# Kernel optimization log

Hardware: AMD Instinct MI355X
Metric: run time of the kernel (lower is better)

The kernel has to match this reference:

```python
import jax, jax.numpy as jnp
import numpy as np

# ---- static physical configuration (matches init_kwargs param dict) ----
NX = NY = 513
NL = 3
N_ENS = 4
LX = LY = 5120.0e3
DX = LX / (NX - 1)
DY = LY / (NY - 1)
F0 = 9.375e-5
BETA = 1.754e-11
A2 = 0.0
A4 = 2.0e9
DELTA_EK = 2.0
TAU0 = 2.0e-5
BCCO = 0.2
ZFBC = BCCO / (1.0 + 0.5 * BCCO)
DT = 600.0
NUM_STEPS = 4
HEIGHTS = np.array([350.0, 750.0, 2900.0])
RED_G = np.array([0.025, 0.0125])

JAC_COEF = 1.0 / (F0 * DX * DY)
HYPERDIFF_COEF = A4 / F0**2 / DX**6
BOTTOM_FRICTION_COEF = DELTA_EK / (2.0 * abs(F0) * DX**2 * (-HEIGHTS[-1]))


def _build_constants():
    """Precompute stratification / mode / Helmholtz matrices (float64 numpy, cast to f32)."""
    A = np.zeros((NL, NL))
    A[0, 0] = 1.0 / (HEIGHTS[0] * RED_G[0])
    A[0, 1] = -1.0 / (HEIGHTS[0] * RED_G[0])
    for i in range(1, NL - 1):
        A[i, i - 1] = -1.0 / (HEIGHTS[i] * RED_G[i - 1])
        A[i, i] = 1.0 / HEIGHTS[i] * (1.0 / RED_G[i] + 1.0 / RED_G[i - 1])
        A[i, i + 1] = -1.0 / (HEIGHTS[i] * RED_G[i])
    A[-1, -1] = 1.0 / (HEIGHTS[NL - 1] * RED_G[NL - 2])
    A[-1, -2] = -1.0 / (HEIGHTS[NL - 1] * RED_G[NL - 2])
    lam_r, R = np.linalg.eig(A)
    lam_l, L = np.linalg.eig(A.T)
    lam_r, R, lam_l, L = lam_r.real, R.real, lam_l.real, L.real
    # align left eigenvectors with right eigenvalue ordering (biorthogonality)
    order = np.array([int(np.argmin(np.abs(lam_l - lr))) for lr in lam_r])
    L = L[:, order]
    Cl2m = np.diag(1.0 / np.diag(L.T @ R)) @ L.T
    Cm2l = R
    lambd = lam_r
    # DST-I eigenvalues of the 5-point Laplacian on the interior grid
    xg, yg = np.meshgrid(np.arange(1, NX - 1), np.arange(1, NY - 1), indexing='ij')
    lap_dst = (2 * (np.cos(np.pi / (NX - 1) * xg) - 1) / DX**2
               + 2 * (np.cos(np.pi / (NY - 1) * yg) - 1) / DY**2)
    helm_dst = lap_dst[None] / F0**2 - lambd[:, None, None]  # (nl, nx-2, ny-2)

    def np_dstI1D(x):
        N = x.shape[-1]
        xp = np.zeros(x.shape[:-1] + (N + 2,))
        xp[..., 1:-1] = x
        return np.fft.irfft(-1j * xp, n=2 * (N + 1), axis=-1, norm='ortho')[..., 1:N + 1]

    def np_dstI2D(x):
        return np.swapaxes(np_dstI1D(np.swapaxes(np_dstI1D(x), -1, -2)), -1, -2)

    const = np.ones((NL, NX, NY)) / (NX * NY)
    s = np.zeros_like(const)
    s[:, 1:-1, 1:-1] = np_dstI2D(np_dstI2D(const[:, 1:-1, 1:-1]) / helm_dst)
    hom_sol = (const + s * lambd[:, None, None])[:-1]  # (nl-1, nx, ny)
    M = (Cm2l[1:] - Cm2l[:-1])[:NL - 1, :NL - 1] * hom_sol.mean((1, 2))[None, :]
    alpha = -np.linalg.inv(M) @ (Cm2l[1:, :-1] - Cm2l[:-1, :-1])
    # wind forcing: curl(tau)/(f0*H1) on interior points; tau_y = 0, tau_x(y) only
    tau_x = -TAU0 * np.cos(2 * np.pi * (np.arange(NY) + 0.5) / NY)[None, :] * np.ones((NX, NY))
    dtaux_dy = (tau_x[1:-1, 2:] - tau_x[1:-1, :-2]) / (2 * DY)
    wind = (-dtaux_dy / (F0 * HEIGHTS[0]))[None]  # (1, nx-2, ny-2)
    f32 = lambda a: jnp.asarray(a, jnp.float32)
    return dict(A=f32(A), Cl2m=f32(Cl2m), Cm2l=f32(Cm2l), helmoltz_dst=f32(helm_dst),
                alpha_matrix=f32(alpha), homogeneous_sol=f32(hom_sol), wind_forcing=f32(wind))


# ---------------- stencil ops ----------------

def _pad11(x):
    return jnp.pad(x, [(0, 0)] * (x.ndim - 2) + [(1, 1), (1, 1)])


def laplacian_h_nobc(f):
    # unscaled 5-point Laplacian, interior values only: (..., nx-2, ny-2)
    return (f[..., 2:, 1:-1] + f[..., :-2, 1:-1] + f[..., 1:-1, 2:] + f[..., 1:-1, :-2]
            - 4.0 * f[..., 1:-1, 1:-1])


def laplacian_h(f, fc):
    # full-grid Laplacian with partial-slip boundary treatment (coefficient fc = zfbc)
    lap = _pad11(laplacian_h_nobc(f))
    lap = lap.at[..., 0, :].set(fc * (f[..., 1, :] - f[..., 0, :]))
    lap = lap.at[..., -1, :].set(fc * (f[..., -2, :] - f[..., -1, :]))
    lap = lap.at[..., :, 0].set(fc * (f[..., :, 1] - f[..., :, 0]))
    lap = lap.at[..., :, -1].set(fc * (f[..., :, -2] - f[..., :, -1]))
    return lap


def laplacian_h_boundaries(f, fc):
    # boundary Laplacian values, concat order: x=0 (y interior), x=-1, y=0 (full x), y=-1
    return jnp.concatenate([
        fc * (f[..., 1, 1:-1] - f[..., 0, 1:-1]),
        fc * (f[..., -2, 1:-1] - f[..., -1, 1:-1]),
        fc * (f[..., :, 1] - f[..., :, 0]),
        fc * (f[..., :, -2] - f[..., :, -1])], axis=-1)


def jacobi_h(f, g):
    # Arakawa 9-point Jacobian J(f, g), interior values (..., nx-2, ny-2)
    dx_f = f[..., 2:, :] - f[..., :-2, :]
    dx_g = g[..., 2:, :] - g[..., :-2, :]
    dy_f = f[..., 2:] - f[..., :-2]
    dy_g = g[..., 2:] - g[..., :-2]
    return ((dx_f[..., 1:-1] * dy_g[..., 1:-1, :] - dx_g[..., 1:-1] * dy_f[..., 1:-1, :])
            + (f[..., 2:, 1:-1] * dy_g[..., 2:, :] - f[..., :-2, 1:-1] * dy_g[..., :-2, :])
            - (f[..., 1:-1, 2:] * dx_g[..., 2:] - f[..., 1:-1, :-2] * dx_g[..., :-2])
            + (g[..., 1:-1, 2:] * dx_f[..., 2:] - g[..., 1:-1, :-2] * dx_f[..., :-2])
            - (g[..., 2:, 1:-1] * dy_f[..., 2:, :] - g[..., :-2, 1:-1] * dy_f[..., :-2, :])) / 12.0


# ---------------- DST-I elliptic solve ----------------

def dstI1D(x):
    N = x.shape[-1]
    z = jnp.zeros(x.shape[:-1] + (1,), x.dtype)
    xp = jnp.concatenate([z, x, z], axis=-1)
    return jnp.fft.irfft(-1j * xp.astype(jnp.complex64), n=2 * (N + 1), axis=-1,
                         norm='ortho')[..., 1:N + 1]


def dstI2D(x):
    return jnp.swapaxes(dstI1D(jnp.swapaxes(dstI1D(x), -1, -2)), -1, -2)


def inverse_elliptic_dst(f, op_dst):
    return dstI2D(dstI2D(f) / op_dst)


# ---------------- QG time derivative ----------------

def _time_derivatives(y, A, Cl2m, Cm2l, helm_dst, alpha, hom_sol, wind):
    q, p = y[0], y[1]  # (..., nl, nx, ny)
    # advection + hyperdiffusion RHS on interior (a_2 == 0 branch skipped as in source)
    rhs = JAC_COEF * jacobi_h(q, p)
    delta2_p = laplacian_h(p, ZFBC)
    rhs = rhs - HYPERDIFF_COEF * laplacian_h_nobc(laplacian_h(delta2_p, ZFBC))
    rhs = rhs.at[..., 0:1, :, :].add(wind)
    rhs = rhs.at[..., -1:, :, :].add(BOTTOM_FRICTION_COEF * laplacian_h_nobc(p[..., -1:, :, :]))
    dq = _pad11(rhs)
    # layers -> modes, DST Helmholtz inversion, homogeneous-solution correction
    rhs_h = jnp.einsum('ij,...jxy->...ixy', Cl2m, dq)
    dp_modes = _pad11(inverse_elliptic_dst(rhs_h[..., 1:-1, 1:-1], helm_dst))
    mean_m = dp_modes[..., :-1, :, :].mean((-2, -1))  # (..., nl-1)
    dalpha = jnp.einsum('ij,...j->...i', alpha, mean_m)[..., None, None]
    dp_modes = dp_modes.at[..., :-1, :, :].add(dalpha * hom_sol)
    dp = jnp.einsum('ij,...jxy->...ixy', Cm2l, dp_modes)
    # boundary vorticity update
    dp_bound = jnp.concatenate([dp[..., 0, 1:-1], dp[..., -1, 1:-1],
                                dp[..., :, 0], dp[..., :, -1]], axis=-1)
    delta_p_bound = laplacian_h_boundaries(dp / (F0 * DX)**2, ZFBC)
    dq_bound = delta_p_bound - jnp.einsum('ij,...jl->...il', A, dp_bound)
    ny2 = NY - 2
    dq = dq.at[..., 0, 1:-1].set(dq_bound[..., :ny2])
    dq = dq.at[..., -1, 1:-1].set(dq_bound[..., ny2:2 * ny2])
    dq = dq.at[..., :, 0].set(dq_bound[..., 2 * ny2:2 * ny2 + NX])
    dq = dq.at[..., :, -1].set(dq_bound[..., 2 * ny2 + NX:2 * ny2 + 2 * NX])
    return jnp.stack((dq, dp), 0)


def _forecast(y0, t, A, Cl2m, Cm2l, helm_dst, alpha, hom_sol, wind):
    deriv = lambda y: _time_derivatives(y, A, Cl2m, Cm2l, helm_dst, alpha, hom_sol, wind)

    def step(y, dt_):
        k1 = deriv(y)
        k2 = deriv(y + 0.5 * dt_ * k1)
        k3 = deriv(y + 0.5 * dt_ * k2)
        k4 = deriv(y + dt_ * k3)
        y_next = y + (dt_ / 6.0) * (k1 + 2.0 * k2 + 2.0 * k3 + k4)
        return y_next, y_next

    _, traj = jax.lax.scan(step, y0, t[1:] - t[:-1])
    return jnp.concatenate([y0[None], traj], axis=0)  # (T, 2, n_ens, nl, nx, ny)


def setup_inputs() -> dict:
    key = jax.random.key(0)
    y0 = 0.1 * jax.random.normal(key, (2, N_ENS, NL, NX, NY), dtype=jnp.float32)
    t = jnp.arange(NUM_STEPS + 1, dtype=jnp.float32) * DT
    consts = _build_constants()
    return dict(y0=y0, t=t, **consts)


def reference(y0, t, A, Cl2m, Cm2l, helmoltz_dst, alpha_matrix, homogeneous_sol, wind_forcing):
    return _forecast(y0, t, A, Cl2m, Cm2l, helmoltz_dst, alpha_matrix,
                     homogeneous_sol, wind_forcing)
```

## Files before the change

### kernel.cpp

```cpp
#include <hip/hip_runtime.h>
#include <math.h>

#define NXY 513
#define NIN 511
#define NL3 3
#define NE4 4
#define NB 12
#define GLD 512

static constexpr long FS  = (long)NE4 * NL3 * NXY * NXY;
static constexpr long GSZ = (long)NB * GLD * GLD;
static constexpr int  NSTEPS = 4;

static constexpr double dF0 = 9.375e-05;
static constexpr double dDX = 10000.0;
static constexpr float ZFBCf     = (float)(0.2 / (1.0 + 0.5 * 0.2));
static constexpr float JACCf     = (float)(1.0 / (dF0 * dDX * dDX));
static constexpr float HYPCf     = (float)(2.0e9 / (dF0 * dF0) / (dDX*dDX*dDX*dDX*dDX*dDX));
static constexpr float BFCf      = (float)(2.0 / (2.0 * dF0 * dDX * dDX * (-2900.0)));
static constexpr float INVF0DX2f = (float)(1.0 / ((dF0 * dDX) * (dF0 * dDX)));

typedef short  bf16x8 __attribute__((ext_vector_type(8)));
typedef float  f32x4  __attribute__((ext_vector_type(4)));
typedef unsigned int u32;
typedef __attribute__((address_space(1))) const u32 GAS;
typedef __attribute__((address_space(3))) u32 LAS;
#define GLDS(gp, lp) __builtin_amdgcn_global_load_lds((GAS*)(gp), (LAS*)(lp), 16, 0, 0)

__device__ __forceinline__ unsigned short f2bf(float x) {
    unsigned int u = __float_as_uint(x);
    return (unsigned short)((u + 0x7FFFu + ((u >> 16) & 1u)) >> 16);
}
__device__ __forceinline__ float bf2f(unsigned short h) {
    return __uint_as_float(((unsigned int)h) << 16);
}

__global__ void initS_kernel(unsigned short* __restrict__ Sh, unsigned short* __restrict__ Sl) {
    int k = blockIdx.x * 256 + threadIdx.x;
    int n = blockIdx.y;
    if (k >= GLD || n >= GLD) return;
    float v = 0.f;
    if (n < NIN && k < NIN) {
        int m = ((n + 1) * (k + 1)) & 1023;
        v = (float)(0.0625 * sin(M_PI * (double)m / 512.0));
    }
    unsigned short hs = f2bf(v);
    Sh[n * GLD + k] = hs;
    Sl[n * GLD + k] = f2bf(v - bf2f(hs));
}

__global__ __launch_bounds__(256) void fused_rhs(
    float* __restrict__ kq, const float* __restrict__ q, const float* __restrict__ p,
    const float* __restrict__ wind)
{
    __shared__ float ps[22][72];
    __shared__ float qs[22][72];
    __shared__ float l1[22][72];
    __shared__ float l2[22][72];
    const int c  = blockIdx.z;
    const int x0 = 1 + blockIdx.y * 16;
    const int y0 = 1 + blockIdx.x * 64;
    const int t  = threadIdx.x;
    const size_t off = (size_t)c * NXY * NXY;
    const float* pp = p + off;
    const float* qp = q + off;

    for (int idx = t; idx < 22 * 70; idx += 256) {
        int i = idx / 70, j = idx % 70;
        int gx = x0 - 3 + i, gy = y0 - 3 + j;
        bool in = (gx >= 0 && gx < NXY && gy >= 0 && gy < NXY);
        size_t go = (size_t)gx * NXY + gy;
        ps[i][j] = in ? pp[go] : 0.f;
        qs[i][j] = in ? qp[go] : 0.f;
    }
    __syncthreads();

#define LAPBC(a, i, j, gx, gy) \
    ((gy) == 0       ? ZFBCf * (a[i][(j)+1] - a[i][j]) : \
     (gy) == NXY-1   ? ZFBCf * (a[i][(j)-1] - a[i][j]) : \
     (gx) == 0       ? ZFBCf * (a[(i)+1][j] - a[i][j]) : \
     (gx) == NXY-1   ? ZFBCf * (a[(i)-1][j] - a[i][j]) : \
     a[(i)+1][j] + a[(i)-1][j] + a[i][(j)+1] + a[i][(j)-1] - 4.f * a[i][j])

    for (int idx = t; idx < 20 * 68; idx += 256) {
        int i = 1 + idx / 68, j = 1 + idx % 68;
        int gx = x0 - 3 + i, gy = y0 - 3 + j;
        float v = 0.f;
        if (gx >= 0 && gx < NXY && gy >= 0 && gy < NXY) v = LAPBC(ps, i, j, gx, gy);
        l1[i][j] = v;
    }
    __syncthreads();

    for (int idx = t; idx < 18 * 66; idx += 256) {
        int i = 2 + idx / 66, j = 2 + idx % 66;
        int gx = x0 - 3 + i, gy = y0 - 3 + j;
        float v = 0.f;
        if (gx >= 0 && gx < NXY && gy >= 0 && gy < NXY) v = LAPBC(l1, i, j, gx, gy);
        l2[i][j] = v;
    }
    __syncthreads();
#undef LAPBC

    const int l = c % NL3;
    for (int idx = t; idx < 16 * 64; idx += 256) {
        int i = 3 + idx / 64, j = 3 + idx % 64;
        int gx = x0 - 3 + i, gy = y0 - 3 + j;
        if (gx > NIN || gy > NIN) continue;
        float fmm=qs[i-1][j-1], fm0=qs[i-1][j], fmp=qs[i-1][j+1];
        float f0m=qs[i][j-1],                    f0p=qs[i][j+1];
        float fpm=qs[i+1][j-1], fp0=qs[i+1][j], fpp=qs[i+1][j+1];
        float gmm=ps[i-1][j-1], gm0=ps[i-1][j], gmp=ps[i-1][j+1];
        float g0m=ps[i][j-1],   g00=ps[i][j],   g0p=ps[i][j+1];
        float gpm=ps[i+1][j-1], gp0=ps[i+1][j], gpp=ps[i+1][j+1];
        float J1 = (fp0 - fm0) * (g0p - g0m) - (gp0 - gm0) * (f0p - f0m);
        float J2 = fp0 * (gpp - gpm) - fm0 * (gmp - gmm);
        float J3 = f0p * (gpp - gmp) - f0m * (gpm - gmm);
        float J4 = g0p * (fpp - fmp) - g0m * (fpm - fmm);
        float J5 = gp0 * (fpp - fpm) - gm0 * (fmp - fmm);
        float jac = (J1 + J2 - J3 + J4 - J5) * (1.0f / 12.0f);
        float lap3 = l2[i+1][j] + l2[i-1][j] + l2[i][j+1] + l2[i][j-1] - 4.f * l2[i][j];
        float v = JACCf * jac - HYPCf * lap3;
        if (l == 0)       v += wind[(size_t)(gx-1) * NIN + (gy-1)];
        if (l == NL3-1)   v += BFCf * (gp0 + gm0 + g0p + g0m - 4.f * g00);
        kq[off + (size_t)gx * NXY + gy] = v;
    }
}

__global__ void l2m_kernel(unsigned short* __restrict__ Gh, unsigned short* __restrict__ Gl,
                           const float* __restrict__ kq, const float* __restrict__ Cl2m) {
    int ry = blockIdx.x * blockDim.x + threadIdx.x;
    int rx = blockIdx.y * blockDim.y + threadIdx.y;
    int e = blockIdx.z;
    size_t go = (size_t)(e * NL3) * GLD * GLD + (size_t)rx * GLD + ry;
    if (rx >= NIN || ry >= NIN) {
        for (int i = 0; i < 3; ++i) { Gh[go + (size_t)i*GLD*GLD] = 0; Gl[go + (size_t)i*GLD*GLD] = 0; }
        return;
    }
    size_t base = ((size_t)(e * NL3) * NXY + (rx + 1)) * NXY + (ry + 1);
    float f0 = kq[base];
    float f1 = kq[base + (size_t)NXY*NXY];
    float f2 = kq[base + 2*(size_t)NXY*NXY];
    float v[3];
    v[0] = Cl2m[0]*f0 + Cl2m[1]*f1 + Cl2m[2]*f2;
    v[1] = Cl2m[3]*f0 + Cl2m[4]*f1 + Cl2m[5]*f2;
    v[2] = Cl2m[6]*f0 + Cl2m[7]*f1 + Cl2m[8]*f2;
#pragma unroll
    for (int i = 0; i < 3; ++i) {
        unsigned short hs = f2bf(v[i]);
        Gh[go + (size_t)i*GLD*GLD] = hs;
        Gl[go + (size_t)i*GLD*GLD] = f2bf(v[i] - bf2f(hs));
    }
}

#define EPLD 133
__global__ __launch_bounds__(256, 2) void gemm_dst(
    const unsigned short* __restrict__ Ah, const unsigned short* __restrict__ Al,
    const unsigned short* __restrict__ Sh, const unsigned short* __restrict__ Sl,
    unsigned short* __restrict__ Ch, unsigned short* __restrict__ Cl,
    float* __restrict__ Cf, const float* __restrict__ helm)
{
    __shared__ __attribute__((aligned(16))) char ldsraw[49152];
    float* ep = (float*)ldsraw;
    const int id = blockIdx.x;
    const int nblk = id / 48, rr = id - nblk * 48;
    const int b = rr >> 2, mblk = rr & 3;
    const int m0 = mblk << 7, n0 = nblk << 6;
    const int t = threadIdx.x;
    const int wave = t >> 6, lane = t & 63;
    const int wr = wave >> 1, wc = wave & 1;
    const int lr = lane & 15, g = lane >> 4;
    const unsigned short* Abh = Ah + (size_t)b * 262144;
    const unsigned short* Abl = Al + (size_t)b * 262144;

    size_t gA[2]; int ldA[2];
#pragma unroll
    for (int u = 0; u < 2; ++u) {
        int o = wave*1024 + u*4096 + lane*16;
        gA[u] = (size_t)(m0 + (o >> 6)) * 512 + ((o & 63) >> 1);
        ldA[u] = wave*1024 + u*4096;
    }
    int oB = wave*1024 + lane*16;
    size_t gB = (size_t)(n0 + (oB >> 6)) * 512 + ((oB & 63) >> 1);
    int ldB = wave*1024;

    auto STAGE = [&](int buf, int kt) {
        char* bb = ldsraw + buf*24576;
        int ke = kt * 32;
#pragma unroll
        for (int u = 0; u < 2; ++u) {
            GLDS(Abh + gA[u] + ke, bb + ldA[u]);
            GLDS(Abl + gA[u] + ke, bb + 8192 + ldA[u]);
        }
        GLDS(Sh + gB + ke, bb + 16384 + ldB);
        GLDS(Sl + gB + ke, bb + 20480 + ldB);
    };

    f32x4 acc[4][2] = {};
    int abyte[4], bbyte[2];
#pragma unroll
    for (int i = 0; i < 4; ++i) abyte[i] = (wr*64 + i*16 + lr)*64 + g*16;
#pragma unroll
    for (int j = 0; j < 2; ++j) bbyte[j] = 16384 + (wc*32 + j*16 + lr)*64 + g*16;

    STAGE(0, 0);
    __syncthreads();
    for (int it = 0; it < 16; ++it) {
        const int buf = it & 1;
        if (it < 15) STAGE(buf ^ 1, it + 1);
        const char* bb = ldsraw + buf*24576;
        bf16x8 fbh[2], fbl[2];
#pragma unroll
        for (int j = 0; j < 2; ++j) {
            fbh[j] = *(const bf16x8*)(bb + bbyte[j]);
            fbl[j] = *(const bf16x8*)(bb + 4096 + bbyte[j]);
        }
#pragma unroll
        for (int i = 0; i < 4; ++i) {
            bf16x8 fah = *(const bf16x8*)(bb + abyte[i]);
            bf16x8 fal = *(const bf16x8*)(bb + 8192 + abyte[i]);
#pragma unroll
            for (int j = 0; j < 2; ++j) {
                acc[i][j] = __builtin_amdgcn_mfma_f32_16x16x32_bf16(fah, fbh[j], acc[i][j], 0, 0, 0);
                acc[i][j] = __builtin_amdgcn_mfma_f32_16x16x32_bf16(fah, fbl[j], acc[i][j], 0, 0, 0);
                acc[i][j] = __builtin_amdgcn_mfma_f32_16x16x32_bf16(fal, fbh[j], acc[i][j], 0, 0, 0);
            }
        }
        __syncthreads();
    }

    const int mode = b % NL3;
    const float* hp = helm ? (helm + (size_t)mode * NIN * NIN) : nullptr;
#pragma unroll
    for (int i = 0; i < 4; ++i) {
        int mml = wr*64 + i*16 + 4*g;
#pragma unroll
        for (int j = 0; j < 2; ++j) {
            int nnl = wc*32 + j*16 + lr;
            int nn = n0 + nnl;
            float v[4];
#pragma unroll
            for (int r = 0; r < 4; ++r) v[r] = acc[i][j][r];
            if (hp && nn < NIN) {
                int mmb = m0 + mml;
#pragma unroll
                for (int r = 0; r < 4; ++r)
                    if (mmb + r < NIN) v[r] /= hp[(size_t)nn*NIN + mmb + r];
            }
#pragma unroll
            for (int r = 0; r < 4; ++r) ep[nnl*EPLD + mml + r] = v[r];
        }
    }
    __syncthreads();

#pragma unroll
    for (int c = 0; c < 4; ++c) {
        int chunk = t + 256*c;
        int row = chunk >> 4;
        int cb  = (chunk & 15) * 8;
        float v[8];
#pragma unroll
        for (int k = 0; k < 8; ++k) v[k] = ep[row*EPLD + cb + k];
        size_t co = (size_t)b*262144 + (size_t)(n0 + row)*512 + m0 + cb;
        if (Cf) {
            f32x4 v0 = {v[0], v[1], v[2], v[3]};
            f32x4 v1 = {v[4], v[5], v[6], v[7]};
            *(f32x4*)(Cf + co)     = v0;
            *(f32x4*)(Cf + co + 4) = v1;
        } else {
            unsigned int h[4], lo[4];
#pragma unroll
            for (int k = 0; k < 4; ++k) {
                unsigned short h0 = f2bf(v[2*k]), h1 = f2bf(v[2*k+1]);
                unsigned short l0 = f2bf(v[2*k]-bf2f(h0)), l1 = f2bf(v[2*k+1]-bf2f(h1));
                h[k]  = (unsigned int)h0 | ((unsigned int)h1 << 16);
                lo[k] = (unsigned int)l0 | ((unsigned int)l1 << 16);
            }
            *(uint4*)(Ch + co) = make_uint4(h[0], h[1], h[2], h[3]);
            *(uint4*)(Cl + co) = make_uint4(lo[0], lo[1], lo[2], lo[3]);
        }
    }
}

__global__ void mean_kernel(float* __restrict__ partial, const float* __restrict__ G) {
    int gy = blockIdx.y;
    int e = gy >> 1, m = gy & 1;
    const float* g = G + (size_t)(e * NL3 + m) * GLD * GLD;
    float s = 0.f;
    for (int idx = blockIdx.x * 256 + threadIdx.x; idx < GLD*GLD; idx += 64 * 256)
        s += g[idx];
    __shared__ float red[256];
    red[threadIdx.x] = s; __syncthreads();
    for (int w = 128; w >= 1; w >>= 1) {
        if (threadIdx.x < w) red[threadIdx.x] += red[threadIdx.x + w];
        __syncthreads();
    }
    if (threadIdx.x == 0) partial[gy * 64 + blockIdx.x] = red[0];
}

__global__ void dalpha_kernel(float* __restrict__ dal, const float* __restrict__ partial,
                              const float* __restrict__ alpha) {
    int t = threadIdx.x;
    if (t >= 8) return;
    int e = t >> 1, i = t & 1;
    float s0 = 0.f, s1 = 0.f;
    for (int bk = 0; bk < 64; ++bk) { s0 += partial[(e*2+0)*64 + bk]; s1 += partial[(e*2+1)*64 + bk]; }
    const float inv = 1.0f / ((float)NXY * (float)NXY);
    dal[t] = alpha[i*2+0] * (s0 * inv) + alpha[i*2+1] * (s1 * inv);
}

__global__ void m2l_kernel(float* __restrict__ kp, const float* __restrict__ G,
                           const float* __restrict__ dal, const float* __restrict__ hom,
                           const float* __restrict__ Cm2l) {
    int y = blockIdx.x * blockDim.x + threadIdx.x;
    int x = blockIdx.y * blockDim.y + threadIdx.y;
    int e = blockIdx.z;
    if (x >= NXY || y >= NXY) return;
    float mv[3];
    bool interior = (x >= 1 && x <= NIN && y >= 1 && y <= NIN);
#pragma unroll
    for (int i = 0; i < 3; ++i)
        mv[i] = interior ? G[(size_t)(e*NL3 + i) * GLD * GLD + (size_t)(x-1) * GLD + (y-1)] : 0.f;
    float h0 = hom[(size_t)x * NXY + y];
    float h1 = hom[(size_t)NXY*NXY + (size_t)x * NXY + y];
    mv[0] += dal[e*2 + 0] * h0;
    mv[1] += dal[e*2 + 1] * h1;
#pragma unroll
    for (int l = 0; l < 3; ++l)
        kp[((size_t)(e*NL3 + l) * NXY + x) * NXY + y] =
            Cm2l[l*3+0]*mv[0] + Cm2l[l*3+1]*mv[1] + Cm2l[l*3+2]*mv[2];
}

__global__ void bound_kernel(float* __restrict__ kq, const float* __restrict__ kp,
                             const float* __restrict__ Amat) {
    int pos = blockIdx.x * 256 + threadIdx.x;
    int e = blockIdx.y;
    if (pos >= 2048) return;
    int x, y, xn, yn;
    if (pos < NIN)            { x = 0;      y = pos + 1;        xn = 1;      yn = y; }
    else if (pos < 2*NIN)     { x = NXY-1;  y = pos - NIN + 1;  xn = NXY-2;  yn = y; }
    else if (pos < 2*NIN+NXY) { x = pos - 2*NIN;       y = 0;      xn = x; yn = 1; }
    else                      { x = pos - (2*NIN+NXY); y = NXY-1;  xn = x; yn = NXY-2; }
    float dpb[3], lpb[3];
#pragma unroll
    for (int j = 0; j < 3; ++j) {
        const float* f = kp + (size_t)(e*NL3 + j) * NXY * NXY;
        float c = f[(size_t)x * NXY + y];
        float nb = f[(size_t)xn * NXY + yn];
        dpb[j] = c;
        lpb[j] = ZFBCf * INVF0DX2f * (nb - c);
    }
#pragma unroll
    for (int l = 0; l < 3; ++l) {
        float v = lpb[l] - (Amat[l*3+0]*dpb[0] + Amat[l*3+1]*dpb[1] + Amat[l*3+2]*dpb[2]);
        kq[((size_t)(e*NL3 + l) * NXY + x) * NXY + y] = v;
    }
}

__global__ void rk_fused(float4* __restrict__ o1, float4* __restrict__ o2,
                         const float4* __restrict__ x, const float4* __restrict__ k,
                         float c1, float c2, int accumulate,
                         const float* __restrict__ t, int s, long n4) {
    float dt = t[s+1] - t[s];
    float a1 = c1 * dt, a2 = c2 * dt;
    for (long i = (long)blockIdx.x * blockDim.x + threadIdx.x; i < n4;
         i += (long)gridDim.x * blockDim.x) {
        float4 kk = k[i], xx = x[i];
        float4 b0 = accumulate ? o1[i] : xx;
        o1[i] = make_float4(b0.x + a1*kk.x, b0.y + a1*kk.y, b0.z + a1*kk.z, b0.w + a1*kk.w);
        if (o2) o2[i] = make_float4(xx.x + a2*kk.x, xx.y + a2*kk.y, xx.z + a2*kk.z, xx.w + a2*kk.w);
    }
}

__global__ void copy_kernel(float4* __restrict__ out, const float4* __restrict__ in, long n4) {
    for (long i = (long)blockIdx.x * blockDim.x + threadIdx.x; i < n4;
         i += (long)gridDim.x * blockDim.x)
        out[i] = in[i];
}

extern "C" void kernel_launch(void* const* d_in, const int* in_sizes, int n_in,
                              void* d_out, int out_size, void* d_ws, size_t ws_size,
                              hipStream_t stream) {
    const float* y0    = (const float*)d_in[0];
    const float* tarr  = (const float*)d_in[1];
    const float* Amat  = (const float*)d_in[2];
    const float* Cl2m  = (const float*)d_in[3];
    const float* Cm2l  = (const float*)d_in[4];
    const float* helm  = (const float*)d_in[5];
    const float* alpha = (const float*)d_in[6];
    const float* hom   = (const float*)d_in[7];
    const float* wind  = (const float*)d_in[8];
    float* out = (float*)d_out;
    char* base = (char*)d_ws;

    unsigned short* Sh = (unsigned short*)base;
    unsigned short* Sl = (unsigned short*)(base + 512*1024);
    float* ytmp = (float*)(base + 1024*1024);
    float* kbuf = ytmp + 2*FS;
    char*  REGb = (char*)(kbuf + 2*FS);
    unsigned short* P0h = (unsigned short*)REGb;
    unsigned short* P0l = P0h + GSZ;
    unsigned short* P1h = P0l + GSZ;
    unsigned short* P1l = P1h + GSZ;
    float* R4 = (float*)REGb;
    float* partial = (float*)(REGb + (size_t)2*FS*sizeof(float));
    float* dal = partial + 512;

    const dim3 bSt(64, 4, 1);
    const dim3 gSt4((NXY + 63)/64, (NXY + 3)/4, NE4);
    const dim3 gL2M(8, 128, NE4);
    const dim3 gF(8, 32, NB);
    const dim3 gG(384, 1, 1);
    const long n4 = 2*FS/4;

    initS_kernel<<<dim3(2, GLD), 256, 0, stream>>>(Sh, Sl);
    copy_kernel<<<1024, 256, 0, stream>>>((float4*)out, (const float4*)y0, n4);

    auto deriv = [&](const float* y, float* k) {
        const float* q = y;  const float* p = y + FS;
        float* kq = k;       float* kp = k + FS;
        fused_rhs<<<gF, 256, 0, stream>>>(kq, q, p, wind);
        l2m_kernel<<<gL2M, bSt, 0, stream>>>(P0h, P0l, kq, Cl2m);
        gemm_dst<<<gG, 256, 0, stream>>>(P0h, P0l, Sh, Sl, P1h, P1l, nullptr, nullptr);
        gemm_dst<<<gG, 256, 0, stream>>>(P1h, P1l, Sh, Sl, P0h, P0l, nullptr, helm);
        gemm_dst<<<gG, 256, 0, stream>>>(P0h, P0l, Sh, Sl, P1h, P1l, nullptr, nullptr);
        gemm_dst<<<gG, 256, 0, stream>>>(P1h, P1l, Sh, Sl, nullptr, nullptr, R4, nullptr);
        mean_kernel<<<dim3(64, 8), 256, 0, stream>>>(partial, R4);
        dalpha_kernel<<<1, 64, 0, stream>>>(dal, partial, alpha);
        m2l_kernel<<<gSt4, bSt, 0, stream>>>(kp, R4, dal, hom, Cm2l);
        bound_kernel<<<dim3(8, NE4), 256, 0, stream>>>(kq, kp, Amat);
    };

    for (int s = 0; s < NSTEPS; ++s) {
        float* ycur  = out + (size_t)s * 2 * FS;
        float* ynext = out + (size_t)(s + 1) * 2 * FS;
        deriv(ycur, kbuf);
        rk_fused<<<1024, 256, 0, stream>>>((float4*)ynext, (float4*)ytmp, (const float4*)ycur,
                                           (const float4*)kbuf, 1.f/6.f, 0.5f, 0, tarr, s, n4);
        deriv(ytmp, kbuf);
        rk_fused<<<1024, 256, 0, stream>>>((float4*)ynext, (float4*)ytmp, (const float4*)ycur,
                                           (const float4*)kbuf, 2.f/6.f, 0.5f, 1, tarr, s, n4);
        deriv(ytmp, kbuf);
        rk_fused<<<1024, 256, 0, stream>>>((float4*)ynext, (float4*)ytmp, (const float4*)ycur,
                                           (const float4*)kbuf, 2.f/6.f, 1.0f, 1, tarr, s, n4);
        deriv(ytmp, kbuf);
        rk_fused<<<1024, 256, 0, stream>>>((float4*)ynext, nullptr, (const float4*)ycur,
                                           (const float4*)kbuf, 1.f/6.f, 0.f, 1, tarr, s, n4);
    }
}
```

Before: 2.283 ms.

## Shrink DST GEMM tile to 64x64 with XOR-swizzled LDS layout

The split-bf16 DST GEMM tile is halved from 128x64 to 64x64, doubling the grid to 768 blocks and cutting LDS per block to 32KB so launch bounds can request 3 blocks per SIMD. The LDS staging layout now uses an XOR swizzle on the 16-byte column chunk to reduce bank conflicts on fragment reads. This aims at better CU occupancy and fill across the 256 CUs, at the cost of less A/B reuse per block and more global traffic for the shared DST matrix.

```diff
diff --git a/kernel.cpp b/kernel.cpp
--- a/kernel.cpp
+++ b/kernel.cpp
@@ -152,19 +152,19 @@
     }
 }
 
-#define EPLD 133
-__global__ __launch_bounds__(256, 2) void gemm_dst(
+#define EPLD 68
+__global__ __launch_bounds__(256, 3) void gemm_dst(
     const unsigned short* __restrict__ Ah, const unsigned short* __restrict__ Al,
     const unsigned short* __restrict__ Sh, const unsigned short* __restrict__ Sl,
     unsigned short* __restrict__ Ch, unsigned short* __restrict__ Cl,
     float* __restrict__ Cf, const float* __restrict__ helm)
 {
-    __shared__ __attribute__((aligned(16))) char ldsraw[49152];
+    __shared__ __attribute__((aligned(16))) char ldsraw[32768];
     float* ep = (float*)ldsraw;
     const int id = blockIdx.x;
-    const int nblk = id / 48, rr = id - nblk * 48;
-    const int b = rr >> 2, mblk = rr & 3;
-    const int m0 = mblk << 7, n0 = nblk << 6;
+    const int nblk = id / 96, rr = id - nblk * 96;
+    const int b = rr >> 3, mblk = rr & 7;
+    const int m0 = mblk << 6, n0 = nblk << 6;
     const int t = threadIdx.x;
     const int wave = t >> 6, lane = t & 63;
     const int wr = wave >> 1, wc = wave & 1;
@@ -172,42 +172,40 @@
     const unsigned short* Abh = Ah + (size_t)b * 262144;
     const unsigned short* Abl = Al + (size_t)b * 262144;
 
-    size_t gA[2]; int ldA[2];
-#pragma unroll
-    for (int u = 0; u < 2; ++u) {
-        int o = wave*1024 + u*4096 + lane*16;
-        gA[u] = (size_t)(m0 + (o >> 6)) * 512 + ((o & 63) >> 1);
-        ldA[u] = wave*1024 + u*4096;
-    }
-    int oB = wave*1024 + lane*16;
-    size_t gB = (size_t)(n0 + (oB >> 6)) * 512 + ((oB & 63) >> 1);
-    int ldB = wave*1024;
+    const int srow = t >> 2;
+    const int scol = ((t & 3) ^ ((srow >> 1) & 3)) * 8;
+    const size_t gAe = (size_t)(m0 + srow) * 512 + scol;
+    const size_t gBe = (size_t)(n0 + srow) * 512 + scol;
+    const int ldbase = wave * 1024;
 
     auto STAGE = [&](int buf, int kt) {
-        char* bb = ldsraw + buf*24576;
+        char* bb = ldsraw + buf * 16384;
         int ke = kt * 32;
-#pragma unroll
-        for (int u = 0; u < 2; ++u) {
-            GLDS(Abh + gA[u] + ke, bb + ldA[u]);
-            GLDS(Abl + gA[u] + ke, bb + 8192 + ldA[u]);
-        }
-        GLDS(Sh + gB + ke, bb + 16384 + ldB);
-        GLDS(Sl + gB + ke, bb + 20480 + ldB);
+        GLDS(Abh + gAe + ke, bb + ldbase);
+        GLDS(Abl + gAe + ke, bb + 4096 + ldbase);
+        GLDS(Sh  + gBe + ke, bb + 8192 + ldbase);
+        GLDS(Sl  + gBe + ke, bb + 12288 + ldbase);
     };
 
-    f32x4 acc[4][2] = {};
-    int abyte[4], bbyte[2];
-#pragma unroll
-    for (int i = 0; i < 4; ++i) abyte[i] = (wr*64 + i*16 + lr)*64 + g*16;
-#pragma unroll
-    for (int j = 0; j < 2; ++j) bbyte[j] = 16384 + (wc*32 + j*16 + lr)*64 + g*16;
+    f32x4 acc[2][2] = {};
+    int abyte[2], bbyte[2];
+#pragma unroll
+    for (int i = 0; i < 2; ++i) {
+        int ar = wr*32 + i*16 + lr;
+        abyte[i] = ar*64 + ((g ^ ((ar >> 1) & 3)) * 16);
+    }
+#pragma unroll
+    for (int j = 0; j < 2; ++j) {
+        int br = wc*32 + j*16 + lr;
+        bbyte[j] = 8192 + br*64 + ((g ^ ((br >> 1) & 3)) * 16);
+    }
 
     STAGE(0, 0);
     __syncthreads();
     for (int it = 0; it < 16; ++it) {
         const int buf = it & 1;
         if (it < 15) STAGE(buf ^ 1, it + 1);
-        const char* bb = ldsraw + buf*24576;
+        const char* bb = ldsraw + buf * 16384;
         bf16x8 fbh[2], fbl[2];
 #pragma unroll
         for (int j = 0; j < 2; ++j) {
@@ -215,9 +213,9 @@
             fbl[j] = *(const bf16x8*)(bb + 4096 + bbyte[j]);
         }
 #pragma unroll
-        for (int i = 0; i < 4; ++i) {
+        for (int i = 0; i < 2; ++i) {
             bf16x8 fah = *(const bf16x8*)(bb + abyte[i]);
-            bf16x8 fal = *(const bf16x8*)(bb + 8192 + abyte[i]);
+            bf16x8 fal = *(const bf16x8*)(bb + 4096 + abyte[i]);
 #pragma unroll
             for (int j = 0; j < 2; ++j) {
                 acc[i][j] = __builtin_amdgcn_mfma_f32_16x16x32_bf16(fah, fbh[j], acc[i][j], 0, 0, 0);
@@ -231,8 +229,8 @@
     const int mode = b % NL3;
     const float* hp = helm ? (helm + (size_t)mode * NIN * NIN) : nullptr;
 #pragma unroll
-    for (int i = 0; i < 4; ++i) {
-        int mml = wr*64 + i*16 + 4*g;
+    for (int i = 0; i < 2; ++i) {
+        int mml = wr*32 + i*16 + 4*g;
 #pragma unroll
         for (int j = 0; j < 2; ++j) {
             int nnl = wc*32 + j*16 + lr;
@@ -253,10 +251,10 @@
     __syncthreads();
 
 #pragma unroll
-    for (int c = 0; c < 4; ++c) {
+    for (int c = 0; c < 2; ++c) {
         int chunk = t + 256*c;
-        int row = chunk >> 4;
-        int cb  = (chunk & 15) * 8;
+        int row = chunk >> 3;
+        int cb  = (chunk & 7) * 8;
         float v[8];
 #pragma unroll
         for (int k = 0; k < 8; ++k) v[k] = ep[row*EPLD + cb + k];
@@ -409,7 +407,7 @@
     const dim3 gSt4((NXY + 63)/64, (NXY + 3)/4, NE4);
     const dim3 gL2M(8, 128, NE4);
     const dim3 gF(8, 32, NB);
-    const dim3 gG(384, 1, 1);
+    const dim3 gG(768, 1, 1);
     const long n4 = 2*FS/4;
 
     initS_kernel<<<dim3(2, GLD), 256, 0, stream>>>(Sh, Sl);
```

After: 2.264 ms. Within noise of the previous version (-0.8%).
